# Kernel tuning notes

Measured on AMD Instinct MI355X. Metric: run time of the kernel, lower is better.

## Reference

```python
import jax, jax.numpy as jnp
import numpy as np

EMBED_DIM = 768
SCALE = float(np.sqrt(EMBED_DIM / 9.0))


def setup_inputs() -> dict:
    key = jax.random.key(0)
    ks = jax.random.split(key, 7)
    D = EMBED_DIM
    s = 1.0 / np.sqrt(D)
    x = jax.random.normal(ks[0], (8, 2048, D), dtype=jnp.float32)
    Wq = jax.random.uniform(ks[1], (D, D), jnp.float32, -s, s)
    bq = jax.random.uniform(ks[2], (D,), jnp.float32, -s, s)
    Wk = jax.random.uniform(ks[3], (D, D), jnp.float32, -s, s)
    bk = jax.random.uniform(ks[4], (D,), jnp.float32, -s, s)
    Wv = jax.random.uniform(ks[5], (D, D), jnp.float32, -s, s)
    bv = jax.random.uniform(ks[6], (D,), jnp.float32, -s, s)
    return {"x": x, "Wq": Wq, "bq": bq, "Wk": Wk, "bk": bk, "Wv": Wv, "bv": bv}


def reference(x, Wq, bq, Wk, bk, Wv, bv):
    # nn.Linear: y = x @ W^T + b
    Q = jnp.einsum('bnd,ed->bne', x, Wq) + bq
    K = jnp.einsum('bnd,ed->bne', x, Wk) + bk
    V = jnp.einsum('bnd,ed->bne', x, Wv) + bv
    scores = jnp.einsum('bqd,bkd->bqk', Q, K) / SCALE  # [B, Nq, Nk]
    # NOTE: softmax over the QUERY axis (dim=-2), per the original module
    weights = jax.nn.softmax(scores, axis=-2)
    out = jnp.einsum('bqk,bkd->bqd', weights, V)
    return out + x
```

## Files before the change

### kernel.cpp

```cpp
#include <hip/hip_runtime.h>
#include <stdint.h>

#define B_ 8
#define N_ 2048
#define D_ 768

typedef unsigned short u16;
typedef unsigned int u32;
typedef __attribute__((ext_vector_type(8))) short bf16x8;
typedef __attribute__((ext_vector_type(8))) unsigned short u16x8;
typedef __attribute__((ext_vector_type(4))) float f32x4;

static constexpr float INV_SCALE = 0.10825317547305482f;

__device__ __forceinline__ u16 f2bf(float f) {
  union { float f; unsigned u; } v; v.f = f;
  return (u16)((v.u + 0x7FFFu + ((v.u >> 16) & 1u)) >> 16);
}
__device__ __forceinline__ float bf2f(u16 h) {
  union { unsigned u; float f; } v; v.u = ((unsigned)h) << 16;
  return v.f;
}
__device__ __forceinline__ f32x4 mfma16(bf16x8 a, bf16x8 b, f32x4 c) {
  return __builtin_amdgcn_mfma_f32_16x16x32_bf16(a, b, c, 0, 0, 0);
}
__device__ __forceinline__ void gl_lds16(const void* g, void* l) {
  __builtin_amdgcn_global_load_lds(
      (const __attribute__((address_space(1))) u32*)g,
      (__attribute__((address_space(3))) u32*)l, 16, 0, 0);
}

__global__ __launch_bounds__(256) void cast_kernel(
    const float* __restrict__ x, const float* __restrict__ wq,
    const float* __restrict__ wk, const float* __restrict__ wv,
    u16* __restrict__ xb, u16* __restrict__ wqb,
    u16* __restrict__ wkb, u16* __restrict__ wvb) {
  const long NX = (long)B_ * N_ * D_;
  const long NW = (long)D_ * D_;
  long i = ((long)blockIdx.x * 256 + threadIdx.x) * 8;
  const float* src; u16* dst; long off;
  if (i < NX) { src = x; dst = xb; off = i; }
  else {
    long j = i - NX;
    int seg = (int)(j / NW);
    off = j - (long)seg * NW;
    src = seg == 0 ? wq : (seg == 1 ? wk : wv);
    dst = seg == 0 ? wqb : (seg == 1 ? wkb : wvb);
  }
  float4 a = *(const float4*)(src + off);
  float4 b = *(const float4*)(src + off + 4);
  u16x8 o;
  o[0]=f2bf(a.x); o[1]=f2bf(a.y); o[2]=f2bf(a.z); o[3]=f2bf(a.w);
  o[4]=f2bf(b.x); o[5]=f2bf(b.y); o[6]=f2bf(b.z); o[7]=f2bf(b.w);
  *(u16x8*)(dst + off) = o;
}

template<int NT, int NF>
__device__ __forceinline__ void gemm256(
    const u16* __restrict__ Ag, long lda,
    const u16* __restrict__ Bg, long ldb,
    f32x4 (&acc)[8][NF]) {
  __shared__ u16 Ab[2][16384];
  __shared__ u16 Bb[2][NF * 4096];
  const int t_ = threadIdx.x, l = t_ & 63, w = t_ >> 6;
  const int lr = l & 15, kq = l >> 4;
  const int wm = w >> 2, wn = w & 3;
  const int arow = wm * 128, brow = wn * (NF * 16);
  const int s_rowl = l >> 3;
  const int s_sl = (l & 7) ^ (l >> 3);
  auto STAGE_A = [&](u16* As, int kt) {
    #pragma unroll
    for (int j = 0; j < 4; ++j) {
      const int row = j * 64 + w * 8 + s_rowl;
      gl_lds16(Ag + (long)row * lda + kt * 64 + s_sl * 8,
               As + ((j * 8192 + w * 1024) >> 1));
    }
  };
  auto STAGE_B = [&](u16* Bs, int kt) {
    #pragma unroll
    for (int j = 0; j < NF; ++j) {
      const int row = j * 64 + w * 8 + s_rowl;
      gl_lds16(Bg + (long)row * ldb + kt * 64 + s_sl * 8,
               Bs + ((j * 8192 + w * 1024) >> 1));
    }
  };

#define TILE(XA, XB, YA, YB, kt, DOST)                                       \
  {                                                                          \
    if (DOST) {                                                              \
      STAGE_A(YA, (kt) + 1);                                                 \
      asm volatile("s_waitcnt vmcnt(4)" ::: "memory");                       \
    } else {                                                                 \
      asm volatile("s_waitcnt vmcnt(0)" ::: "memory");                       \
    }                                                                        \
    __builtin_amdgcn_s_barrier();                                            \
    asm volatile("" ::: "memory");                                           \
    bf16x8 bf[NF][2];                                                        \
    _Pragma("unroll")                                                        \
    for (int nf = 0; nf < NF; ++nf) {                                        \
      const int row = brow + nf * 16 + lr;                                   \
      _Pragma("unroll")                                                      \
      for (int ks = 0; ks < 2; ++ks)                                         \
        bf[nf][ks] = *(const bf16x8*)(XB + row * 64 +                        \
                        (((4 * ks + kq) ^ (lr & 7)) * 8));                   \
    }                                                                        \
    {                                                                        \
      bf16x8 af[4][2];                                                       \
      _Pragma("unroll")                                                      \
      for (int mf = 0; mf < 4; ++mf) {                                       \
        const int row = arow + mf * 16 + lr;                                 \
        _Pragma("unroll")                                                    \
        for (int ks = 0; ks < 2; ++ks)                                       \
          af[mf][ks] = *(const bf16x8*)(XA + row * 64 +                      \
                          (((4 * ks + kq) ^ (lr & 7)) * 8));                 \
      }                                                                      \
      __builtin_amdgcn_s_setprio(1);                                         \
      _Pragma("unroll")                                                      \
      for (int ks = 0; ks < 2; ++ks)                                         \
        _Pragma("unroll")                                                    \
        for (int mf = 0; mf < 4; ++mf)                                       \
          _Pragma("unroll")                                                  \
          for (int nf = 0; nf < NF; ++nf)                                    \
            acc[mf][nf] = mfma16(af[mf][ks], bf[nf][ks], acc[mf][nf]);       \
      __builtin_amdgcn_s_setprio(0);                                         \
    }                                                                        \
    if (DOST) STAGE_B(YB, (kt) + 1);                                         \
    {                                                                        \
      bf16x8 af[4][2];                                                       \
      _Pragma("unroll")                                                      \
      for (int mf = 0; mf < 4; ++mf) {                                       \
        const int row = arow + 64 + mf * 16 + lr;                            \
        _Pragma("unroll")                                                    \
        for (int ks = 0; ks < 2; ++ks)                                       \
          af[mf][ks] = *(const bf16x8*)(XA + row * 64 +                      \
                          (((4 * ks + kq) ^ (lr & 7)) * 8));                 \
      }                                                                      \
      __builtin_amdgcn_s_setprio(1);                                         \
      _Pragma("unroll")                                                      \
      for (int ks = 0; ks < 2; ++ks)                                         \
        _Pragma("unroll")                                                    \
        for (int mf = 0; mf < 4; ++mf)                                       \
          _Pragma("unroll")                                                  \
          for (int nf = 0; nf < NF; ++nf)                                    \
            acc[4 + mf][nf] = mfma16(af[mf][ks], bf[nf][ks], acc[4 + mf][nf]); \
      __builtin_amdgcn_s_setprio(0);                                         \
    }                                                                        \
    asm volatile("" ::: "memory");                                           \
    __builtin_amdgcn_s_barrier();                                            \
  }

  STAGE_A(Ab[0], 0);
  STAGE_B(Bb[0], 0);
  for (int t2 = 0; t2 < NT; t2 += 2) {
    TILE(Ab[0], Bb[0], Ab[1], Bb[1], t2, true)
    TILE(Ab[1], Bb[1], Ab[0], Bb[0], t2 + 1, (t2 + 2 < NT))
  }
#undef TILE
}

__global__ __launch_bounds__(512, 1) void qkv_gemm(
    const u16* __restrict__ xb,
    const u16* __restrict__ wq, const u16* __restrict__ wk, const u16* __restrict__ wv,
    const float* __restrict__ bq, const float* __restrict__ bk, const float* __restrict__ bv,
    u16* __restrict__ Qs, u16* __restrict__ Kb, u16* __restrict__ Vb) {
  const int lin = blockIdx.x;
  const int xcd = lin & 7, inner = lin >> 3;
  const int rt = xcd * 8 + (inner & 7);
  const int ct = inner >> 3;
  const int mat = ct >> 2;
  const u16* W = mat == 0 ? wq : (mat == 1 ? wk : wv);
  const float* bias = mat == 0 ? bq : (mat == 1 ? bk : bv);
  u16* out = mat == 0 ? Qs : (mat == 1 ? Kb : Vb);
  const float scl = mat == 0 ? INV_SCALE : 1.0f;
  const int rbase = rt * 256, cbase = (ct & 3) * 192;

  f32x4 acc[8][3] = {};
  gemm256<D_ / 64, 3>(xb + (long)rbase * D_, D_, W + (long)cbase * D_, D_, acc);

  const int l = threadIdx.x & 63, w = threadIdx.x >> 6;
  const int lr = l & 15, orow = (l >> 4) * 4;
  const int wm = w >> 2, wn = w & 3;
  #pragma unroll
  for (int mf = 0; mf < 8; ++mf)
    #pragma unroll
    for (int nf = 0; nf < 3; ++nf) {
      int col = cbase + wn * 48 + nf * 16 + lr;
      float bc = bias[col];
      #pragma unroll
      for (int r = 0; r < 4; ++r) {
        int row = rbase + wm * 128 + mf * 16 + orow + r;
        out[(long)row * D_ + col] = f2bf((acc[mf][nf][r] + bc) * scl);
      }
    }
}

__global__ __launch_bounds__(512, 1) void qk_exp(
    const u16* __restrict__ Qs, const u16* __restrict__ Kb,
    u16* __restrict__ P, float* __restrict__ denpart) {
  const int lin = blockIdx.x;
  const int b = lin & 7, inner = lin >> 3;
  const int kblk = inner & 7, qblk = inner >> 3;

  f32x4 acc[8][4] = {};
  gemm256<D_ / 64, 4>(Qs + ((long)b * N_ + qblk * 256) * D_, D_,
                      Kb + ((long)b * N_ + kblk * 256) * D_, D_, acc);

  const int tt = threadIdx.x, l = tt & 63, w = tt >> 6;
  const int lr = l & 15, orow = (l >> 4) * 4;
  const int wm = w >> 2, wn = w & 3;
  float csum[4] = {0.f, 0.f, 0.f, 0.f};
  #pragma unroll
  for (int mf = 0; mf < 8; ++mf)
    #pragma unroll
    for (int nf = 0; nf < 4; ++nf) {
      long kk = kblk * 256 + wn * 64 + nf * 16 + lr;
      #pragma unroll
      for (int r = 0; r < 4; ++r) {
        long q = qblk * 256 + wm * 128 + mf * 16 + orow + r;
        float e = __expf(acc[mf][nf][r]);
        u16 pe = f2bf(e);
        P[((long)b * N_ + q) * N_ + kk] = pe;
        csum[nf] += bf2f(pe);
      }
    }
  #pragma unroll
  for (int nf = 0; nf < 4; ++nf) {
    csum[nf] += __shfl_xor(csum[nf], 16);
    csum[nf] += __shfl_xor(csum[nf], 32);
  }
  if (l < 16) {
    #pragma unroll
    for (int nf = 0; nf < 4; ++nf)
      denpart[((long)(qblk * 2 + wm) * B_ + b) * N_ +
              kblk * 256 + wn * 64 + nf * 16 + l] = csum[nf];
  }
}

__global__ __launch_bounds__(256) void scale_transpose(
    const u16* __restrict__ Vb, const float* __restrict__ denpart,
    u16* __restrict__ VsT) {
  const int b = blockIdx.z, k0 = blockIdx.y * 64, d0 = blockIdx.x * 64;
  __shared__ float tile[64][65];
  __shared__ float invden[64];
  const int t = threadIdx.x;
  if (t < 64) {
    float s = 0.f;
    for (int qs = 0; qs < 16; ++qs)
      s += denpart[((long)qs * B_ + b) * N_ + k0 + t];
    invden[t] = 1.0f / s;
  }
  __syncthreads();
  for (int idx = t; idx < 4096; idx += 256) {
    int kl = idx >> 6, dl = idx & 63;
    float v = bf2f(Vb[((long)b * N_ + k0 + kl) * D_ + d0 + dl]) * invden[kl];
    tile[dl][kl] = v;
  }
  __syncthreads();
  for (int idx = t; idx < 4096; idx += 256) {
    int dl = idx >> 6, kl = idx & 63;
    VsT[((long)b * D_ + d0 + dl) * N_ + k0 + kl] = f2bf(tile[dl][kl]);
  }
}

__global__ __launch_bounds__(512, 1) void pv_gemm(
    const u16* __restrict__ P, const u16* __restrict__ VsT,
    const u16* __restrict__ xb, float* __restrict__ out) {
  const int lin = blockIdx.x;
  const int b = lin & 7, inner = lin >> 3;
  const int qt = inner & 7, dt = inner >> 3;
  const int q0 = qt * 256, d0 = dt * 192;

  f32x4 acc[8][3] = {};
  gemm256<N_ / 64, 3>(P + ((long)b * N_ + q0) * N_, N_,
                      VsT + ((long)b * D_ + d0) * N_, N_, acc);

  const int l = threadIdx.x & 63, w = threadIdx.x >> 6;
  const int lr = l & 15, orow = (l >> 4) * 4;
  const int wm = w >> 2, wn = w & 3;
  #pragma unroll
  for (int mf = 0; mf < 8; ++mf)
    #pragma unroll
    for (int nf = 0; nf < 3; ++nf) {
      int dd = d0 + wn * 48 + nf * 16 + lr;
      #pragma unroll
      for (int r = 0; r < 4; ++r) {
        int q = q0 + wm * 128 + mf * 16 + orow + r;
        long idx = ((long)b * N_ + q) * D_ + dd;
        out[idx] = acc[mf][nf][r] + bf2f(xb[idx]);
      }
    }
}

extern "C" void kernel_launch(void* const* d_in, const int* in_sizes, int n_in,
                              void* d_out, int out_size, void* d_ws, size_t ws_size,
                              hipStream_t stream) {
  const float* x  = (const float*)d_in[0];
  const float* Wq = (const float*)d_in[1];
  const float* bq = (const float*)d_in[2];
  const float* Wk = (const float*)d_in[3];
  const float* bk = (const float*)d_in[4];
  const float* Wv = (const float*)d_in[5];
  const float* bv = (const float*)d_in[6];

  char* ws = (char*)d_ws;
  u16* xb  = (u16*)(ws + 0);
  u16* wqb = (u16*)(ws + 25165824);
  u16* wkb = (u16*)(ws + 26345472);
  u16* wvb = (u16*)(ws + 27525120);
  u16* Qs  = (u16*)(ws + 28704768);
  u16* Kb  = (u16*)(ws + 53870592);
  u16* Vb  = (u16*)(ws + 79036416);
  u16* VsT = (u16*)(ws + 104202240);
  u16* P   = (u16*)(ws + 129368064);
  float* denpart = (float*)(ws + 196476928);
  (void)in_sizes; (void)n_in; (void)out_size; (void)ws_size;

  cast_kernel<<<7008, 256, 0, stream>>>(x, Wq, Wk, Wv, xb, wqb, wkb, wvb);
  qkv_gemm<<<768, 512, 0, stream>>>(xb, wqb, wkb, wvb, bq, bk, bv, Qs, Kb, Vb);
  qk_exp<<<512, 512, 0, stream>>>(Qs, Kb, P, denpart);
  scale_transpose<<<dim3(12, 32, 8), 256, 0, stream>>>(Vb, denpart, VsT);
  pv_gemm<<<256, 512, 0, stream>>>(P, VsT, xb, (float*)d_out);
}
```

Before: 209.8 us.

## Split GEMM tile into four barrier-separated LDS-read/MFMA phases

```diff
diff --git a/kernel.cpp b/kernel.cpp
--- a/kernel.cpp
+++ b/kernel.cpp
@@ -85,6 +85,31 @@
     }
   };
 
+#define RD_AF(XA, MF0, AF)                                                   \
+    _Pragma("unroll")                                                        \
+    for (int mf = 0; mf < 2; ++mf) {                                         \
+      const int row = arow + ((MF0) + mf) * 16 + lr;                         \
+      _Pragma("unroll")                                                      \
+      for (int ks = 0; ks < 2; ++ks)                                         \
+        AF[mf][ks] = *(const bf16x8*)(XA + row * 64 +                        \
+                        (((4 * ks + kq) ^ (lr & 7)) * 8));                   \
+    }
+
+#define PH_MFMA(MF0, AF)                                                     \
+    asm volatile("s_waitcnt lgkmcnt(0)" ::: "memory");                       \
+    __builtin_amdgcn_s_setprio(1);                                           \
+    _Pragma("unroll")                                                        \
+    for (int ks = 0; ks < 2; ++ks)                                           \
+      _Pragma("unroll")                                                      \
+      for (int mf = 0; mf < 2; ++mf)                                         \
+        _Pragma("unroll")                                                    \
+        for (int nf = 0; nf < NF; ++nf)                                      \
+          acc[(MF0) + mf][nf] =                                              \
+              mfma16(AF[mf][ks], bf[nf][ks], acc[(MF0) + mf][nf]);           \
+    __builtin_amdgcn_s_setprio(0);                                           \
+    asm volatile("" ::: "memory");                                           \
+    __builtin_amdgcn_s_barrier();
+
 #define TILE(XA, XB, YA, YB, kt, DOST)                                       \
   {                                                                          \
     if (DOST) {                                                              \
@@ -104,49 +129,27 @@
         bf[nf][ks] = *(const bf16x8*)(XB + row * 64 +                        \
                         (((4 * ks + kq) ^ (lr & 7)) * 8));                   \
     }                                                                        \
-    {                                                                        \
-      bf16x8 af[4][2];                                                       \
-      _Pragma("unroll")                                                      \
-      for (int mf = 0; mf < 4; ++mf) {                                       \
-        const int row = arow + mf * 16 + lr;                                 \
-        _Pragma("unroll")                                                    \
-        for (int ks = 0; ks < 2; ++ks)                                       \
-          af[mf][ks] = *(const bf16x8*)(XA + row * 64 +                      \
-                          (((4 * ks + kq) ^ (lr & 7)) * 8));                 \
-      }                                                                      \
-      __builtin_amdgcn_s_setprio(1);                                         \
-      _Pragma("unroll")                                                      \
-      for (int ks = 0; ks < 2; ++ks)                                         \
-        _Pragma("unroll")                                                    \
-        for (int mf = 0; mf < 4; ++mf)                                       \
-          _Pragma("unroll")                                                  \
-          for (int nf = 0; nf < NF; ++nf)                                    \
-            acc[mf][nf] = mfma16(af[mf][ks], bf[nf][ks], acc[mf][nf]);       \
-      __builtin_amdgcn_s_setprio(0);                                         \
-    }                                                                        \
+    bf16x8 af01[2][2];                                                       \
+    RD_AF(XA, 0, af01);                                                      \
+    asm volatile("" ::: "memory");                                           \
+    __builtin_amdgcn_s_barrier();                                            \
+    PH_MFMA(0, af01)                                                         \
+    bf16x8 af23[2][2];                                                       \
+    RD_AF(XA, 2, af23);                                                      \
     if (DOST) STAGE_B(YB, (kt) + 1);                                         \
-    {                                                                        \
-      bf16x8 af[4][2];                                                       \
-      _Pragma("unroll")                                                      \
-      for (int mf = 0; mf < 4; ++mf) {                                       \
-        const int row = arow + 64 + mf * 16 + lr;                            \
-        _Pragma("unroll")                                                    \
-        for (int ks = 0; ks < 2; ++ks)                                       \
-          af[mf][ks] = *(const bf16x8*)(XA + row * 64 +                      \
-                          (((4 * ks + kq) ^ (lr & 7)) * 8));                 \
-      }                                                                      \
-      __builtin_amdgcn_s_setprio(1);                                         \
-      _Pragma("unroll")                                                      \
-      for (int ks = 0; ks < 2; ++ks)                                         \
-        _Pragma("unroll")                                                    \
-        for (int mf = 0; mf < 4; ++mf)                                       \
-          _Pragma("unroll")                                                  \
-          for (int nf = 0; nf < NF; ++nf)                                    \
-            acc[4 + mf][nf] = mfma16(af[mf][ks], bf[nf][ks], acc[4 + mf][nf]); \
-      __builtin_amdgcn_s_setprio(0);                                         \
-    }                                                                        \
-    asm volatile("" ::: "memory");                                           \
-    __builtin_amdgcn_s_barrier();                                            \
+    asm volatile("" ::: "memory");                                           \
+    __builtin_amdgcn_s_barrier();                                            \
+    PH_MFMA(2, af23)                                                         \
+    bf16x8 af45[2][2];                                                       \
+    RD_AF(XA, 4, af45);                                                      \
+    asm volatile("" ::: "memory");                                           \
+    __builtin_amdgcn_s_barrier();                                            \
+    PH_MFMA(4, af45)                                                         \
+    bf16x8 af67[2][2];                                                       \
+    RD_AF(XA, 6, af67);                                                      \
+    asm volatile("" ::: "memory");                                           \
+    __builtin_amdgcn_s_barrier();                                            \
+    PH_MFMA(6, af67)                                                         \
   }
 
   STAGE_A(Ab[0], 0);
@@ -156,6 +159,8 @@
     TILE(Ab[1], Bb[1], Ab[0], Bb[0], t2 + 1, (t2 + 2 < NT))
   }
 #undef TILE
+#undef PH_MFMA
+#undef RD_AF
 }
 
 __global__ __launch_bounds__(512, 1) void qkv_gemm(
```

New measurement: 224.2 us. +6.8%, slower.
